# Kernel tuning notes

Measured on AMD Instinct MI355X. Metric: run time of the kernel, lower is better.

Reference implementation:

```python
import jax, jax.numpy as jnp
import numpy as np

B, N, S, VC, P, E, H = 8, 1024, 64, 8, 3, 64, 4
HD = E // H


def setup_inputs() -> dict:
    key = jax.random.key(0)
    ks = jax.random.split(key, 20)
    def rn(k, shape, scale=1.0):
        return jax.random.normal(k, shape, dtype=jnp.float32) * scale
    inp = {
        "s": rn(ks[0], (B, N, S)),
        "v": rn(ks[1], (B, N, VC, 3)),
        "coords": rn(ks[2], (B, N, 3)),
        # p-adic encoder: Linear(1,16) -> SiLU -> Linear(16, 64)
        "enc_w1": rn(ks[3], (16, 1), 1.0),
        "enc_b1": jnp.zeros((16,), jnp.float32),
        "enc_w2": rn(ks[4], (S, 16), 1.0 / np.sqrt(16)),
        "enc_b2": jnp.zeros((S,), jnp.float32),
        # 3 GVP layers, all with s_cat dim 72 -> s_out 64, v 8 -> 8
        "scal_w": rn(ks[5], (3, S, S + VC), 1.0 / np.sqrt(S + VC)),
        "scal_b": jnp.zeros((3, S), jnp.float32),
        "vec_w": rn(ks[6], (3, VC, VC), 1.0 / np.sqrt(VC)),
        "gate_w": rn(ks[7], (3, VC, S + VC), 1.0 / np.sqrt(S + VC)),
        "gate_b": jnp.zeros((3, VC), jnp.float32),
        # MultiheadAttention (embed 64, 4 heads)
        "in_proj_w": rn(ks[8], (3 * E, E), 1.0 / np.sqrt(E)),
        "in_proj_b": jnp.zeros((3 * E,), jnp.float32),
        "out_proj_w": rn(ks[9], (E, E), 1.0 / np.sqrt(E)),
        "out_proj_b": jnp.zeros((E,), jnp.float32),
    }
    return inp


def _padic_distance(coords):
    # pairwise diffs (B, N, N, 3)
    diff = coords[:, :, None, :] - coords[:, None, :, :]
    di = (jnp.abs(diff) * 1000.0).astype(jnp.int32)
    # valuation = max k in [1,10] with p^k | di  == count of divisible k (divisibility chain)
    cnt = jnp.zeros(di.shape, jnp.int32)
    for k in range(1, 11):
        cnt = cnt + (di % (P ** k) == 0).astype(jnp.int32)
    val = jnp.where(di > 0, cnt, 0).astype(jnp.float32).mean(-1)  # (B,N,N)
    return jnp.float32(P) ** (-val)


def reference(s, v, coords, enc_w1, enc_b1, enc_w2, enc_b2,
              scal_w, scal_b, vec_w, gate_w, gate_b,
              in_proj_w, in_proj_b, out_proj_w, out_proj_b):
    silu = jax.nn.silu
    pd = _padic_distance(coords)  # (B,N,N)
    pf = silu(pd.mean(-1, keepdims=True) @ enc_w1.T + enc_b1) @ enc_w2.T + enc_b2
    s = s + pf

    for i in range(3):
        act = i < 2  # last layer has no activations (gate always applied)
        vn = jnp.linalg.norm(v, axis=-1)               # (B,N,VC)
        sc = jnp.concatenate([s, vn], axis=-1)         # (B,N,S+VC)
        s_new = sc @ scal_w[i].T + scal_b[i]
        if act:
            s_new = silu(s_new)
        v_new = jnp.einsum('oi,bnix->bnox', vec_w[i], v)
        if act:
            v_new = v_new * jax.nn.sigmoid(jnp.linalg.norm(v_new, axis=-1, keepdims=True))
        gate = jax.nn.sigmoid(sc @ gate_w[i].T + gate_b[i])
        v_new = v_new * gate[..., None]
        if i > 0:
            s, v = s + s_new, v + v_new
        else:
            s, v = s_new, v_new

    # p-adic biased multi-head attention (additive mask = -padic_dist per head)
    qkv = s @ in_proj_w.T + in_proj_b                 # (B,N,3E)
    q, k, vv = jnp.split(qkv, 3, axis=-1)
    q = q.reshape(B, N, H, HD)
    k = k.reshape(B, N, H, HD)
    vv = vv.reshape(B, N, H, HD)
    scores = jnp.einsum('bqhd,bkhd->bhqk', q, k) / np.sqrt(HD)
    scores = scores - pd[:, None, :, :]
    attn = jax.nn.softmax(scores, axis=-1)
    o = jnp.einsum('bhqk,bkhd->bqhd', attn, vv).reshape(B, N, E)
    s = s + (o @ out_proj_w.T + out_proj_b)

    return s, v, pd
```

## Files before the change

### kernel.cpp

```cpp
#include <hip/hip_runtime.h>
#include <hip/hip_bf16.h>
#include <math.h>

#define BB 8
#define NN 1024
#define SS 64
#define VCC 8
#define EE 64
#define HH 4
#define HDD 16

#define OUT_S_OFF 0
#define OUT_V_OFF 524288
#define OUT_PD_OFF 720896

__device__ __forceinline__ int val3(int d) {
    int c = 0;
    unsigned ud = (unsigned)d;
    c += (ud % 3u == 0u);
    c += (ud % 9u == 0u);
    c += (ud % 27u == 0u);
    c += (ud % 81u == 0u);
    c += (ud % 243u == 0u);
    c += (ud % 729u == 0u);
    c += (ud % 2187u == 0u);
    c += (ud % 6561u == 0u);
    c += (ud % 19683u == 0u);
    c += (ud % 59049u == 0u);
    return d > 0 ? c : 0;
}

__device__ __forceinline__ float silu_f(float x) {
    return x / (1.0f + expf(-x));
}
__device__ __forceinline__ float sigmoid_f(float x) {
    return 1.0f / (1.0f + expf(-x));
}

#define IR 16
__global__ __launch_bounds__(256) void pd_kernel(const float* __restrict__ coords,
                                                 float* __restrict__ pd_out,
                                                 float* __restrict__ pdmean) {
    const int bi = blockIdx.x;
    const int b = bi >> 6;
    const int ibase = (bi & 63) * IR;
    const int tid = threadIdx.x;
    const float* cb = coords + (size_t)b * NN * 3;

    __shared__ float sx[1024];
    __shared__ float sy[1024];
    __shared__ float sz[1024];
    __shared__ float red[IR][4];

    for (int idx = tid; idx < 3072; idx += 256) {
        float v = cb[idx];
        int j = idx / 3;
        int c = idx - j * 3;
        float* dst = (c == 0) ? sx : (c == 1) ? sy : sz;
        dst[j] = v;
    }
    __syncthreads();

    const int j0 = tid * 4;
    float4 x4 = *(const float4*)&sx[j0];
    float4 y4 = *(const float4*)&sy[j0];
    float4 z4 = *(const float4*)&sz[j0];
    float xs[4] = {x4.x, x4.y, x4.z, x4.w};
    float ys[4] = {y4.x, y4.y, y4.z, y4.w};
    float zs[4] = {z4.x, z4.y, z4.z, z4.w};

    const float kLog2_3_over3 = 0.5283208335737187f;

    for (int ii = 0; ii < IR; ++ii) {
        const int i = ibase + ii;
        const float cx = sx[i], cy = sy[i], cz = sz[i];
        float p[4];
        float lsum = 0.0f;
        #pragma unroll
        for (int t = 0; t < 4; ++t) {
            int d0 = (int)(fabsf(cx - xs[t]) * 1000.0f);
            int d1 = (int)(fabsf(cy - ys[t]) * 1000.0f);
            int d2 = (int)(fabsf(cz - zs[t]) * 1000.0f);
            int cnt = val3(d0) + val3(d1) + val3(d2);
            p[t] = exp2f(-(float)cnt * kLog2_3_over3);
            lsum += p[t];
        }
        *(float4*)&pd_out[((size_t)(b * NN + i)) * NN + j0] =
            make_float4(p[0], p[1], p[2], p[3]);
        float x = lsum;
        #pragma unroll
        for (int off = 32; off > 0; off >>= 1) x += __shfl_xor(x, off, 64);
        if ((tid & 63) == 0) red[ii][tid >> 6] = x;
    }
    __syncthreads();
    if (tid < IR) {
        pdmean[b * NN + ibase + tid] =
            (red[tid][0] + red[tid][1] + red[tid][2] + red[tid][3]) * (1.0f / 1024.0f);
    }
}

#define GR 4
__global__ __launch_bounds__(64) void gvp_kernel(const float* __restrict__ s_in,
                           const float* __restrict__ v_in,
                           const float* __restrict__ enc_w1,
                           const float* __restrict__ enc_b1,
                           const float* __restrict__ enc_w2,
                           const float* __restrict__ enc_b2,
                           const float* __restrict__ scal_w,
                           const float* __restrict__ scal_b,
                           const float* __restrict__ vec_w,
                           const float* __restrict__ gate_w,
                           const float* __restrict__ gate_b,
                           const float* __restrict__ pdmean,
                           float* __restrict__ s_gvp,
                           float* __restrict__ v_out) {
    const int lane = threadIdx.x;
    const int rbase = blockIdx.x * GR;

    __shared__ float sc[GR][80];
    __shared__ float vbuf[GR][24];
    __shared__ float vtb[GR][24];
    __shared__ float gg[GR][8];
    __shared__ float hid[GR][16];

    const int gc = lane >> 3;
    const int gi = lane & 7;

    float gw[3][9];
    #pragma unroll
    for (int L = 0; L < 3; ++L) {
        const float* gwr = gate_w + ((size_t)L * 8 + gc) * 72 + gi;
        #pragma unroll
        for (int t = 0; t < 9; ++t) gw[L][t] = gwr[8 * t];
    }

    #pragma unroll
    for (int r = 0; r < GR; ++r) {
        const int row = rbase + r;
        sc[r][lane] = s_in[(size_t)row * 64 + lane];
        if (lane < 24) vbuf[r][lane] = v_in[(size_t)row * 24 + lane];
        if (lane < 16) {
            float pm = pdmean[row];
            hid[r][lane] = silu_f(pm * enc_w1[lane] + enc_b1[lane]);
        }
    }
    __syncthreads();
    #pragma unroll
    for (int r = 0; r < GR; ++r) {
        float acc = enc_b2[lane];
        #pragma unroll
        for (int h = 0; h < 16; ++h) acc += hid[r][h] * enc_w2[lane * 16 + h];
        sc[r][lane] += acc;
    }
    __syncthreads();

    for (int layer = 0; layer < 3; ++layer) {
        const bool act = layer < 2;
        if (lane < 8) {
            #pragma unroll
            for (int r = 0; r < GR; ++r) {
                float x = vbuf[r][lane * 3 + 0];
                float y = vbuf[r][lane * 3 + 1];
                float z = vbuf[r][lane * 3 + 2];
                sc[r][64 + lane] = sqrtf(x * x + y * y + z * z);
            }
        }
        __syncthreads();

        float sn[GR];
        {
            float4 w4[18];
            const float4* wr = (const float4*)(scal_w + ((size_t)layer * 64 + lane) * 72);
            #pragma unroll
            for (int k = 0; k < 18; ++k) w4[k] = wr[k];
            const float sb = scal_b[layer * 64 + lane];
            #pragma unroll
            for (int r = 0; r < GR; ++r) {
                const float4* sv = (const float4*)sc[r];
                float acc = sb;
                #pragma unroll
                for (int k = 0; k < 18; ++k) {
                    float4 s4 = sv[k];
                    acc += w4[k].x * s4.x + w4[k].y * s4.y + w4[k].z * s4.z + w4[k].w * s4.w;
                }
                sn[r] = acc;
            }
        }
        {
            const float gb = gate_b[layer * 8 + gc];
            #pragma unroll
            for (int r = 0; r < GR; ++r) {
                float ga = 0.0f;
                #pragma unroll
                for (int t = 0; t < 9; ++t) ga += gw[layer][t] * sc[r][gi + 8 * t];
                ga += __shfl_xor(ga, 1, 8);
                ga += __shfl_xor(ga, 2, 8);
                ga += __shfl_xor(ga, 4, 8);
                if (gi == 0) gg[r][gc] = sigmoid_f(ga + gb);
            }
        }
        if (lane < 24) {
            const int o = lane / 3;
            const int xc = lane - o * 3;
            const float* vw = vec_w + ((size_t)layer * 8 + o) * 8;
            float vwr[8];
            #pragma unroll
            for (int ii = 0; ii < 8; ++ii) vwr[ii] = vw[ii];
            #pragma unroll
            for (int r = 0; r < GR; ++r) {
                float acc = 0.0f;
                #pragma unroll
                for (int ii = 0; ii < 8; ++ii) acc += vwr[ii] * vbuf[r][ii * 3 + xc];
                vtb[r][lane] = acc;
            }
        }
        __syncthreads();

        #pragma unroll
        for (int r = 0; r < GR; ++r) {
            float val = act ? silu_f(sn[r]) : sn[r];
            sc[r][lane] = (layer > 0) ? (sc[r][lane] + val) : val;
        }
        if (lane < 24) {
            const int o = lane / 3;
            #pragma unroll
            for (int r = 0; r < GR; ++r) {
                float val = vtb[r][lane];
                if (act) {
                    float a = vtb[r][o * 3 + 0];
                    float bb2 = vtb[r][o * 3 + 1];
                    float c2 = vtb[r][o * 3 + 2];
                    val *= sigmoid_f(sqrtf(a * a + bb2 * bb2 + c2 * c2));
                }
                val *= gg[r][o];
                vbuf[r][lane] = (layer > 0) ? (vbuf[r][lane] + val) : val;
            }
        }
        __syncthreads();
    }

    #pragma unroll
    for (int r = 0; r < GR; ++r) {
        const int row = rbase + r;
        s_gvp[(size_t)row * 64 + lane] = sc[r][lane];
        if (lane < 24) v_out[(size_t)row * 24 + lane] = vbuf[r][lane];
    }
}

#define QROWS 16
__global__ __launch_bounds__(192) void qkv_kernel(const float* __restrict__ s_gvp,
                           const float* __restrict__ w,
                           const float* __restrict__ bias,
                           float* __restrict__ q,
                           float* __restrict__ k,
                           float* __restrict__ v) {
    const int tid = threadIdx.x;
    const int rbase = blockIdx.x * QROWS;
    __shared__ float sl[QROWS][64];
    for (int idx = tid; idx < QROWS * 64; idx += 192)
        sl[idx >> 6][idx & 63] = s_gvp[(size_t)rbase * 64 + idx];
    __syncthreads();

    float4 w4[16];
    const float4* wr = (const float4*)(w + (size_t)tid * 64);
    #pragma unroll
    for (int kk = 0; kk < 16; ++kk) w4[kk] = wr[kk];
    const float bv = bias[tid];

    const int which = tid >> 6;
    const int e = tid & 63;
    const int h = e >> 4, d = e & 15;
    float* dst = (which == 0) ? q : (which == 1) ? k : v;

    #pragma unroll
    for (int r = 0; r < QROWS; ++r) {
        const float4* sv = (const float4*)sl[r];
        float acc = bv;
        #pragma unroll
        for (int kk = 0; kk < 16; ++kk) {
            float4 s4 = sv[kk];
            acc += w4[kk].x * s4.x + w4[kk].y * s4.y + w4[kk].z * s4.z + w4[kk].w * s4.w;
        }
        const int row = rbase + r;
        const int b = row >> 10, n = row & 1023;
        dst[(((size_t)(b * HH + h)) * NN + n) * HDD + d] = acc;
    }
}

__global__ __launch_bounds__(256, 2)
void attn_kernel(const float* __restrict__ q,
                 const float* __restrict__ k,
                 const float* __restrict__ v,
                 const float* __restrict__ pd,
                 float* __restrict__ po,
                 float* __restrict__ pm,
                 float* __restrict__ pl) {
    const int ks = blockIdx.x & 1;
    const int qt = (blockIdx.x >> 1) & 15;
    const int bh = blockIdx.x >> 5;
    const int b = bh >> 2;
    const int tid = threadIdx.x;
    const int kl = tid & 15;
    const int qg = tid >> 4;
    const int qbase = qt * 64 + qg * 4;

    __shared__ float kt[128][20];
    __shared__ float vt[128][20];

    float qreg[4][16];
    const float* qb_ = q + ((size_t)bh * NN + qbase) * HDD;
    #pragma unroll
    for (int i = 0; i < 4; ++i) {
        #pragma unroll
        for (int d = 0; d < 16; d += 4) {
            float4 t4 = *(const float4*)(qb_ + i * 16 + d);
            qreg[i][d] = t4.x; qreg[i][d+1] = t4.y; qreg[i][d+2] = t4.z; qreg[i][d+3] = t4.w;
        }
    }
    const float* pdr0 = pd + ((size_t)b * NN + qbase) * NN + ks * 512;

    float acc[4][16];
    #pragma unroll
    for (int i = 0; i < 4; ++i)
        #pragma unroll
        for (int d = 0; d < 16; ++d) acc[i][d] = 0.0f;
    float mrun[4] = {-INFINITY, -INFINITY, -INFINITY, -INFINITY};
    float lrun[4] = {0.0f, 0.0f, 0.0f, 0.0f};

    const float* kbase = k + ((size_t)bh * NN + ks * 512) * HDD;
    const float* vbase = v + ((size_t)bh * NN + ks * 512) * HDD;
    const float kLog2e = 1.44269504f;

    const int r0 = tid >> 2, s0 = tid & 3;
    const int r1 = (tid + 256) >> 2, s1 = tid & 3;

    float4 kp0, kp1, vp0, vp1;
    {
        const float4* kg = (const float4*)kbase;
        const float4* vg = (const float4*)vbase;
        kp0 = kg[tid]; kp1 = kg[tid + 256];
        vp0 = vg[tid]; vp1 = vg[tid + 256];
    }

    for (int tile = 0; tile < 4; ++tile) {
        __syncthreads();
        *(float4*)&kt[r0][s0 * 4] = kp0;
        *(float4*)&kt[r1][s1 * 4] = kp1;
        *(float4*)&vt[r0][s0 * 4] = vp0;
        *(float4*)&vt[r1][s1 * 4] = vp1;
        __syncthreads();

        if (tile < 3) {
            const float4* kg = (const float4*)(kbase + (size_t)(tile + 1) * 2048);
            const float4* vg = (const float4*)(vbase + (size_t)(tile + 1) * 2048);
            kp0 = kg[tid]; kp1 = kg[tid + 256];
            vp0 = vg[tid]; vp1 = vg[tid + 256];
        }

        float sc[4][8];
        #pragma unroll
        for (int m = 0; m < 8; ++m) {
            const int jt = kl + 16 * m;
            float kr[16];
            #pragma unroll
            for (int d = 0; d < 16; d += 4) {
                float4 t4 = *(const float4*)&kt[jt][d];
                kr[d] = t4.x; kr[d+1] = t4.y; kr[d+2] = t4.z; kr[d+3] = t4.w;
            }
            const int j = tile * 128 + jt;
            #pragma unroll
            for (int i = 0; i < 4; ++i) {
                float a = 0.0f;
                #pragma unroll
                for (int d = 0; d < 16; ++d) a += qreg[i][d] * kr[d];
                sc[i][m] = a * 0.25f - pdr0[(size_t)i * NN + j];
            }
        }

        #pragma unroll
        for (int i = 0; i < 4; ++i) {
            float tmax = sc[i][0];
            #pragma unroll
            for (int m = 1; m < 8; ++m) tmax = fmaxf(tmax, sc[i][m]);
            #pragma unroll
            for (int w = 1; w < 16; w <<= 1) tmax = fmaxf(tmax, __shfl_xor(tmax, w, 16));
            float mnew = fmaxf(mrun[i], tmax);
            float scale = exp2f((mrun[i] - mnew) * kLog2e);
            mrun[i] = mnew;
            lrun[i] *= scale;
            #pragma unroll
            for (int d = 0; d < 16; ++d) acc[i][d] *= scale;
            float ls = 0.0f;
            #pragma unroll
            for (int m = 0; m < 8; ++m) {
                float p = exp2f((sc[i][m] - mnew) * kLog2e);
                sc[i][m] = p;
                ls += p;
            }
            lrun[i] += ls;
        }

        #pragma unroll
        for (int m = 0; m < 8; ++m) {
            const int jt = kl + 16 * m;
            float vr[16];
            #pragma unroll
            for (int d = 0; d < 16; d += 4) {
                float4 t4 = *(const float4*)&vt[jt][d];
                vr[d] = t4.x; vr[d+1] = t4.y; vr[d+2] = t4.z; vr[d+3] = t4.w;
            }
            #pragma unroll
            for (int i = 0; i < 4; ++i) {
                const float p = sc[i][m];
                #pragma unroll
                for (int d = 0; d < 16; ++d) acc[i][d] += p * vr[d];
            }
        }
    }

    #pragma unroll
    for (int i = 0; i < 4; ++i) {
        float l = lrun[i];
        #pragma unroll
        for (int w = 1; w < 16; w <<= 1) l += __shfl_xor(l, w, 16);
        lrun[i] = l;
    }
    float outv[4] = {0.0f, 0.0f, 0.0f, 0.0f};
    #pragma unroll
    for (int i = 0; i < 4; ++i) {
        #pragma unroll
        for (int d = 0; d < 16; ++d) {
            float a = acc[i][d];
            #pragma unroll
            for (int w = 1; w < 16; w <<= 1) a += __shfl_xor(a, w, 16);
            if (kl == d) outv[i] = a;
        }
    }
    const size_t sbase = (size_t)ks * 32768 + (size_t)bh * NN + qbase;
    #pragma unroll
    for (int i = 0; i < 4; ++i) {
        po[(sbase + i) * 16 + kl] = outv[i];
        if (kl == 0) {
            pm[sbase + i] = mrun[i];
            pl[sbase + i] = lrun[i];
        }
    }
}

#define OROWS 16
__global__ __launch_bounds__(256) void outproj_kernel(const float* __restrict__ s_gvp,
                               const float* __restrict__ po,
                               const float* __restrict__ pm,
                               const float* __restrict__ pl,
                               const float* __restrict__ w,
                               const float* __restrict__ bias,
                               float* __restrict__ s_out) {
    const int tid = threadIdx.x;
    const int col = tid & 63;
    const int wq = tid >> 6;
    const int rbase = blockIdx.x * OROWS;
    __shared__ float ol[OROWS][64];
    const float kLog2e = 1.44269504f;
    for (int idx = tid; idx < OROWS * 64; idx += 256) {
        const int r = idx >> 6;
        const int c = idx & 63;
        const int row = rbase + r;
        const int b = row >> 10, n = row & 1023;
        const int h = c >> 4, d = c & 15;
        const size_t i2 = (size_t)(b * HH + h) * NN + n;
        float m0 = pm[i2], m1 = pm[32768 + i2];
        float l0 = pl[i2], l1 = pl[32768 + i2];
        float a0 = po[i2 * 16 + d], a1 = po[(32768 + i2) * 16 + d];
        float mm = fmaxf(m0, m1);
        float e0 = exp2f((m0 - mm) * kLog2e);
        float e1 = exp2f((m1 - mm) * kLog2e);
        ol[r][c] = (a0 * e0 + a1 * e1) / (l0 * e0 + l1 * e1);
    }
    __syncthreads();

    float4 w4[16];
    const float4* wr = (const float4*)(w + (size_t)col * 64);
    #pragma unroll
    for (int kk = 0; kk < 16; ++kk) w4[kk] = wr[kk];
    const float bv = bias[col];

    #pragma unroll
    for (int rr = 0; rr < OROWS / 4; ++rr) {
        const int r = wq * (OROWS / 4) + rr;
        const float4* sv = (const float4*)ol[r];
        float acc = bv;
        #pragma unroll
        for (int kk = 0; kk < 16; ++kk) {
            float4 s4 = sv[kk];
            acc += w4[kk].x * s4.x + w4[kk].y * s4.y + w4[kk].z * s4.z + w4[kk].w * s4.w;
        }
        const int row = rbase + r;
        s_out[(size_t)row * 64 + col] = s_gvp[(size_t)row * 64 + col] + acc;
    }
}

extern "C" void kernel_launch(void* const* d_in, const int* in_sizes, int n_in,
                              void* d_out, int out_size, void* d_ws, size_t ws_size,
                              hipStream_t stream) {
    const float* s_in      = (const float*)d_in[0];
    const float* v_in      = (const float*)d_in[1];
    const float* coords    = (const float*)d_in[2];
    const float* enc_w1    = (const float*)d_in[3];
    const float* enc_b1    = (const float*)d_in[4];
    const float* enc_w2    = (const float*)d_in[5];
    const float* enc_b2    = (const float*)d_in[6];
    const float* scal_w    = (const float*)d_in[7];
    const float* scal_b    = (const float*)d_in[8];
    const float* vec_w     = (const float*)d_in[9];
    const float* gate_w    = (const float*)d_in[10];
    const float* gate_b    = (const float*)d_in[11];
    const float* in_proj_w = (const float*)d_in[12];
    const float* in_proj_b = (const float*)d_in[13];
    const float* out_proj_w= (const float*)d_in[14];
    const float* out_proj_b= (const float*)d_in[15];

    float* out_s  = (float*)d_out + OUT_S_OFF;
    float* out_v  = (float*)d_out + OUT_V_OFF;
    float* out_pd = (float*)d_out + OUT_PD_OFF;

    float* ws      = (float*)d_ws;
    float* pdmean  = ws;
    float* s_gvp   = ws + 8192;
    float* qb      = s_gvp + 524288;
    float* kb      = qb + 524288;
    float* vvb     = kb + 524288;
    float* po      = vvb + 524288;
    float* pm      = po + 2 * 32768 * 16;
    float* pl      = pm + 2 * 32768;

    const int rows = BB * NN;

    pd_kernel<<<BB * (NN / IR), 256, 0, stream>>>(coords, out_pd, pdmean);
    gvp_kernel<<<rows / GR, 64, 0, stream>>>(s_in, v_in, enc_w1, enc_b1, enc_w2, enc_b2,
                                             scal_w, scal_b, vec_w, gate_w, gate_b,
                                             pdmean, s_gvp, out_v);
    qkv_kernel<<<rows / QROWS, 192, 0, stream>>>(s_gvp, in_proj_w, in_proj_b, qb, kb, vvb);
    attn_kernel<<<BB * HH * (NN / 64) * 2, 256, 0, stream>>>(qb, kb, vvb, out_pd, po, pm, pl);
    outproj_kernel<<<rows / OROWS, 256, 0, stream>>>(s_gvp, po, pm, pl,
                                                     out_proj_w, out_proj_b, out_s);
}
```

Before: 176.1 us.

## Drop split-K attention, double-buffer K/V tiles, use lazy per-lane softmax rescale

The attention kernel no longer splits the key range across two blocks. Each block now walks all 1024 keys with double-buffered shared-memory K/V tiles, and the normalized output is written directly, so outproj no longer merges partial results. Online softmax keeps a per-lane running max that is rescaled only when it grows by more than 8, and the cross-lane max reduction is deferred to the end. This removes the partial-buffer traffic and the per-tile shuffles. The cost is half as many attention blocks, which lowers parallelism. The qkv row tile also grows from 16 to 32.

```diff
diff --git a/kernel.cpp b/kernel.cpp
--- a/kernel.cpp
+++ b/kernel.cpp
@@ -247,7 +247,7 @@
     }
 }
 
-#define QROWS 16
+#define QROWS 32
 __global__ __launch_bounds__(192) void qkv_kernel(const float* __restrict__ s_gvp,
                            const float* __restrict__ w,
                            const float* __restrict__ bias,
@@ -292,20 +292,18 @@
                  const float* __restrict__ k,
                  const float* __restrict__ v,
                  const float* __restrict__ pd,
-                 float* __restrict__ po,
-                 float* __restrict__ pm,
-                 float* __restrict__ pl) {
-    const int ks = blockIdx.x & 1;
-    const int qt = (blockIdx.x >> 1) & 15;
-    const int bh = blockIdx.x >> 5;
+                 float* __restrict__ o) {
+    const int bh = blockIdx.x >> 4;
+    const int qt = blockIdx.x & 15;
     const int b = bh >> 2;
+    const int h = bh & 3;
     const int tid = threadIdx.x;
     const int kl = tid & 15;
     const int qg = tid >> 4;
     const int qbase = qt * 64 + qg * 4;
 
-    __shared__ float kt[128][20];
-    __shared__ float vt[128][20];
+    __shared__ float kt[2][128][20];
+    __shared__ float vt[2][128][20];
 
     float qreg[4][16];
     const float* qb_ = q + ((size_t)bh * NN + qbase) * HDD;
@@ -317,7 +315,7 @@
             qreg[i][d] = t4.x; qreg[i][d+1] = t4.y; qreg[i][d+2] = t4.z; qreg[i][d+3] = t4.w;
         }
     }
-    const float* pdr0 = pd + ((size_t)b * NN + qbase) * NN + ks * 512;
+    const float* pdr0 = pd + ((size_t)b * NN + qbase) * NN;
 
     float acc[4][16];
     #pragma unroll
@@ -327,34 +325,35 @@
     float mrun[4] = {-INFINITY, -INFINITY, -INFINITY, -INFINITY};
     float lrun[4] = {0.0f, 0.0f, 0.0f, 0.0f};
 
-    const float* kbase = k + ((size_t)bh * NN + ks * 512) * HDD;
-    const float* vbase = v + ((size_t)bh * NN + ks * 512) * HDD;
+    const float4* kg = (const float4*)(k + (size_t)bh * NN * HDD);
+    const float4* vg = (const float4*)(v + (size_t)bh * NN * HDD);
     const float kLog2e = 1.44269504f;
 
     const int r0 = tid >> 2, s0 = tid & 3;
-    const int r1 = (tid + 256) >> 2, s1 = tid & 3;
-
-    float4 kp0, kp1, vp0, vp1;
-    {
-        const float4* kg = (const float4*)kbase;
-        const float4* vg = (const float4*)vbase;
-        kp0 = kg[tid]; kp1 = kg[tid + 256];
-        vp0 = vg[tid]; vp1 = vg[tid + 256];
-    }
-
-    for (int tile = 0; tile < 4; ++tile) {
-        __syncthreads();
-        *(float4*)&kt[r0][s0 * 4] = kp0;
-        *(float4*)&kt[r1][s1 * 4] = kp1;
-        *(float4*)&vt[r0][s0 * 4] = vp0;
-        *(float4*)&vt[r1][s1 * 4] = vp1;
-        __syncthreads();
-
-        if (tile < 3) {
-            const float4* kg = (const float4*)(kbase + (size_t)(tile + 1) * 2048);
-            const float4* vg = (const float4*)(vbase + (size_t)(tile + 1) * 2048);
-            kp0 = kg[tid]; kp1 = kg[tid + 256];
-            vp0 = vg[tid]; vp1 = vg[tid + 256];
+    const int r1 = r0 + 64;
+
+    float4 kp0 = kg[tid], kp1 = kg[tid + 256];
+    float4 vp0 = vg[tid], vp1 = vg[tid + 256];
+    *(float4*)&kt[0][r0][s0 * 4] = kp0;
+    *(float4*)&kt[0][r1][s0 * 4] = kp1;
+    *(float4*)&vt[0][r0][s0 * 4] = vp0;
+    *(float4*)&vt[0][r1][s0 * 4] = vp1;
+    kp0 = kg[512 + tid]; kp1 = kg[512 + tid + 256];
+    vp0 = vg[512 + tid]; vp1 = vg[512 + tid + 256];
+    __syncthreads();
+
+    for (int t = 0; t < 8; ++t) {
+        const int cur = t & 1;
+        if (t < 7) {
+            *(float4*)&kt[cur ^ 1][r0][s0 * 4] = kp0;
+            *(float4*)&kt[cur ^ 1][r1][s0 * 4] = kp1;
+            *(float4*)&vt[cur ^ 1][r0][s0 * 4] = vp0;
+            *(float4*)&vt[cur ^ 1][r1][s0 * 4] = vp1;
+            if (t < 6) {
+                const int base = (t + 2) * 512;
+                kp0 = kg[base + tid]; kp1 = kg[base + tid + 256];
+                vp0 = vg[base + tid]; vp1 = vg[base + tid + 256];
+            }
         }
 
         float sc[4][8];
@@ -364,10 +363,10 @@
             float kr[16];
             #pragma unroll
             for (int d = 0; d < 16; d += 4) {
-                float4 t4 = *(const float4*)&kt[jt][d];
+                float4 t4 = *(const float4*)&kt[cur][jt][d];
                 kr[d] = t4.x; kr[d+1] = t4.y; kr[d+2] = t4.z; kr[d+3] = t4.w;
             }
-            const int j = tile * 128 + jt;
+            const int j = t * 128 + jt;
             #pragma unroll
             for (int i = 0; i < 4; ++i) {
                 float a = 0.0f;
@@ -382,18 +381,17 @@
             float tmax = sc[i][0];
             #pragma unroll
             for (int m = 1; m < 8; ++m) tmax = fmaxf(tmax, sc[i][m]);
-            #pragma unroll
-            for (int w = 1; w < 16; w <<= 1) tmax = fmaxf(tmax, __shfl_xor(tmax, w, 16));
-            float mnew = fmaxf(mrun[i], tmax);
-            float scale = exp2f((mrun[i] - mnew) * kLog2e);
-            mrun[i] = mnew;
-            lrun[i] *= scale;
-            #pragma unroll
-            for (int d = 0; d < 16; ++d) acc[i][d] *= scale;
+            if (tmax > mrun[i] + 8.0f) {
+                float scale = exp2f((mrun[i] - tmax) * kLog2e);
+                lrun[i] *= scale;
+                #pragma unroll
+                for (int d = 0; d < 16; ++d) acc[i][d] *= scale;
+                mrun[i] = tmax;
+            }
             float ls = 0.0f;
             #pragma unroll
             for (int m = 0; m < 8; ++m) {
-                float p = exp2f((sc[i][m] - mnew) * kLog2e);
+                float p = exp2f((sc[i][m] - mrun[i]) * kLog2e);
                 sc[i][m] = p;
                 ls += p;
             }
@@ -406,7 +404,7 @@
             float vr[16];
             #pragma unroll
             for (int d = 0; d < 16; d += 4) {
-                float4 t4 = *(const float4*)&vt[jt][d];
+                float4 t4 = *(const float4*)&vt[cur][jt][d];
                 vr[d] = t4.x; vr[d+1] = t4.y; vr[d+2] = t4.z; vr[d+3] = t4.w;
             }
             #pragma unroll
@@ -416,42 +414,33 @@
                 for (int d = 0; d < 16; ++d) acc[i][d] += p * vr[d];
             }
         }
+        __syncthreads();
     }
 
     #pragma unroll
     for (int i = 0; i < 4; ++i) {
-        float l = lrun[i];
+        float mg = mrun[i];
+        #pragma unroll
+        for (int w = 1; w < 16; w <<= 1) mg = fmaxf(mg, __shfl_xor(mg, w, 16));
+        const float sc8 = exp2f((mrun[i] - mg) * kLog2e);
+        float l = lrun[i] * sc8;
         #pragma unroll
         for (int w = 1; w < 16; w <<= 1) l += __shfl_xor(l, w, 16);
-        lrun[i] = l;
-    }
-    float outv[4] = {0.0f, 0.0f, 0.0f, 0.0f};
-    #pragma unroll
-    for (int i = 0; i < 4; ++i) {
+        float outv = 0.0f;
         #pragma unroll
         for (int d = 0; d < 16; ++d) {
-            float a = acc[i][d];
+            float a = acc[i][d] * sc8;
             #pragma unroll
             for (int w = 1; w < 16; w <<= 1) a += __shfl_xor(a, w, 16);
-            if (kl == d) outv[i] = a;
-        }
-    }
-    const size_t sbase = (size_t)ks * 32768 + (size_t)bh * NN + qbase;
-    #pragma unroll
-    for (int i = 0; i < 4; ++i) {
-        po[(sbase + i) * 16 + kl] = outv[i];
-        if (kl == 0) {
-            pm[sbase + i] = mrun[i];
-            pl[sbase + i] = lrun[i];
-        }
+            if (kl == d) outv = a;
+        }
+        o[((size_t)(b * NN + qbase + i)) * EE + h * HDD + kl] = outv / l;
     }
 }
 
 #define OROWS 16
 __global__ __launch_bounds__(256) void outproj_kernel(const float* __restrict__ s_gvp,
-                               const float* __restrict__ po,
-                               const float* __restrict__ pm,
-                               const float* __restrict__ pl,
+                               const float* __restrict__ o,
                                const float* __restrict__ w,
                                const float* __restrict__ bias,
                                float* __restrict__ s_out) {
@@ -460,22 +449,8 @@
     const int wq = tid >> 6;
     const int rbase = blockIdx.x * OROWS;
     __shared__ float ol[OROWS][64];
-    const float kLog2e = 1.44269504f;
-    for (int idx = tid; idx < OROWS * 64; idx += 256) {
-        const int r = idx >> 6;
-        const int c = idx & 63;
-        const int row = rbase + r;
-        const int b = row >> 10, n = row & 1023;
-        const int h = c >> 4, d = c & 15;
-        const size_t i2 = (size_t)(b * HH + h) * NN + n;
-        float m0 = pm[i2], m1 = pm[32768 + i2];
-        float l0 = pl[i2], l1 = pl[32768 + i2];
-        float a0 = po[i2 * 16 + d], a1 = po[(32768 + i2) * 16 + d];
-        float mm = fmaxf(m0, m1);
-        float e0 = exp2f((m0 - mm) * kLog2e);
-        float e1 = exp2f((m1 - mm) * kLog2e);
-        ol[r][c] = (a0 * e0 + a1 * e1) / (l0 * e0 + l1 * e1);
-    }
+    for (int idx = tid; idx < OROWS * 64; idx += 256)
+        ol[idx >> 6][idx & 63] = o[(size_t)rbase * 64 + idx];
     __syncthreads();
 
     float4 w4[16];
@@ -529,9 +504,7 @@
     float* qb      = s_gvp + 524288;
     float* kb      = qb + 524288;
     float* vvb     = kb + 524288;
-    float* po      = vvb + 524288;
-    float* pm      = po + 2 * 32768 * 16;
-    float* pl      = pm + 2 * 32768;
+    float* ob      = vvb + 524288;
 
     const int rows = BB * NN;
 
@@ -540,7 +513,6 @@
                                              scal_w, scal_b, vec_w, gate_w, gate_b,
                                              pdmean, s_gvp, out_v);
     qkv_kernel<<<rows / QROWS, 192, 0, stream>>>(s_gvp, in_proj_w, in_proj_b, qb, kb, vvb);
-    attn_kernel<<<BB * HH * (NN / 64) * 2, 256, 0, stream>>>(qb, kb, vvb, out_pd, po, pm, pl);
-    outproj_kernel<<<rows / OROWS, 256, 0, stream>>>(s_gvp, po, pm, pl,
-                                                     out_proj_w, out_proj_b, out_s);
-}
+    attn_kernel<<<BB * HH * (NN / 64), 256, 0, stream>>>(qb, kb, vvb, out_pd, ob);
+    outproj_kernel<<<rows / OROWS, 256, 0, stream>>>(s_gvp, ob, out_proj_w, out_proj_b, out_s);
+}
```

Measured after the change: 224.6 us. +27.6%, slower.
